# Performance work log

Hardware: AMD Instinct MI355X
Metric: run time of the kernel (lower is better)

## Reference

```python
import jax, jax.numpy as jnp
import numpy as np

V, L, H, D = 2048, 16, 8, 64   # vocab, max_chars, n_head, word_vec_d
B = 8192                        # number of words in batch (rows of char_code)
NW_TOTAL = 8192                 # len(word_code)
N_NAMES = 2048                  # total names (4 words each)
N_GROUPS = 8                    # groups of names (256 each)
PAD = 0
TEMP = D ** 0.5
LN_EPS = 1e-5


def make_pos():
    freq = D // 2
    inv = 1.0 / np.power(10000.0, np.arange(freq) / freq)
    ph = np.outer(np.arange(L), inv)
    return jnp.asarray(np.hstack([np.cos(ph), np.sin(ph)]).astype(np.float32))


def setup_inputs() -> dict:
    key = jax.random.key(0)
    ks = jax.random.split(key, 8)
    char_emb = jax.random.normal(ks[0], (V, D), jnp.float32) * 0.02
    char_emb = char_emb.at[PAD].set(0.0)  # padding_idx row
    Wc = jax.random.normal(ks[1], (D, 3 * H * D), jnp.float32) * 0.02
    bc = jnp.zeros((3 * H * D,), jnp.float32)
    Wp = jax.random.normal(ks[2], (D, 3 * H * D), jnp.float32) * 0.02
    bp = jnp.zeros((3 * H * D,), jnp.float32)
    gamma = jnp.ones((D,), jnp.float32)
    beta = jnp.zeros((D,), jnp.float32)
    W1 = jax.random.normal(ks[3], (H, 16), jnp.float32) * 0.1
    b1 = jnp.zeros((16,), jnp.float32)
    W2 = jax.random.normal(ks[4], (16, 8), jnp.float32) * 0.1
    b2 = jnp.zeros((8,), jnp.float32)
    char_code = jax.random.randint(ks[5], (B, L), 1, V)
    char_code = char_code.at[::4, -2:].set(PAD)  # some padded tails
    word_code = jax.random.randint(ks[6], (NW_TOTAL,), 0, B)
    n_words = np.full((N_NAMES,), NW_TOTAL // N_NAMES, dtype=np.int64)
    n_names = np.full((N_GROUPS,), N_NAMES // N_GROUPS, dtype=np.int64)
    return {"char_emb": char_emb, "Wc": Wc, "bc": bc, "Wp": Wp, "bp": bp,
            "gamma": gamma, "beta": beta, "W1": W1, "b1": b1, "W2": W2, "b2": b2,
            "char_code": char_code, "word_code": word_code,
            "n_words": n_words, "n_names": n_names}


def reference(char_emb, Wc, bc, Wp, bp, gamma, beta, W1, b1, W2, b2,
              char_code, word_code, n_words, n_names):
    pos = make_pos()
    # ComputeQKV: linear d -> 3*H*d, reshape [N,3,H,D]
    cqkv = (char_emb @ Wc + bc).reshape(V, 3, H, D)
    cq, ck, cv = cqkv[:, 0], cqkv[:, 1], cqkv[:, 2]        # [V,H,D]
    pqkv = (pos @ Wp + bp).reshape(L, 3, H, D)
    pq, pk, pv = pqkv[:, 0], pqkv[:, 1], pqkv[:, 2]        # [L,H,D]
    # precomputed score tables
    char_qk = jnp.einsum('xhd,yhd->hxy', cq, ck).at[:, :, PAD].set(-1e9)  # [H,V,V]
    pos_qk = jnp.einsum('xhd,yhd->hxy', pq, pk)                            # [H,L,L]
    # char_q@pos_k + (pos_q@char_k)^T summed over the first dim of char_pos_qk
    cp = jnp.einsum('vhd,lhd->hvl', cq, pk) + jnp.einsum('lhd,vhd->hvl', pq, ck)  # [H,V,L]
    code = char_code                                        # [B,L]
    # gather-assembled scores, no [H,B*L,V] intermediate
    sim = (char_qk[:, code[:, :, None], code[:, None, :]]   # [H,B,L,L]
           + cp[:, code]
           + pos_qk[:, None]) / TEMP
    attn = jax.nn.softmax(sim, axis=-1)                     # [H,B,L,L] (dropout=0)
    v = jnp.transpose(cv[code], (2, 0, 1, 3)) + pv.transpose(1, 0, 2)[:, None]  # [H,B,L,D]
    out = jnp.einsum('hbij,hbjd->bihd', attn, v)            # [B,L,H,D]
    mu = out.mean(-1, keepdims=True)
    var = out.var(-1, keepdims=True)
    out = (out - mu) / jnp.sqrt(var + LN_EPS) * gamma + beta  # LayerNorm(D)
    char_ft = jnp.transpose(out, (0, 2, 1, 3))              # [B,H,L,D]
    mask = (code != PAD)
    pooled = jnp.einsum('bl,bhld->bhd', mask.astype(out.dtype), char_ft) \
             / mask.sum(-1)[:, None, None]                  # masked mean over chars
    x = jnp.transpose(pooled, (0, 2, 1))                    # [B,D,H]
    x = jax.nn.relu(x @ W1 + b1) @ W2 + b2                  # MLP over head dim -> [B,D,8]
    word_ft = x.reshape(B, -1)[word_code]                   # [NW_TOTAL, D*8]
    nw = np.asarray(n_words)
    seg = jnp.asarray(np.repeat(np.arange(nw.size), nw))
    name_ft = jax.ops.segment_sum(word_ft, seg, num_segments=nw.size) \
              / jnp.asarray(nw, word_ft.dtype)[:, None]     # ragged mean -> [N_NAMES, D*8]
    splits = np.cumsum(np.asarray(n_names))[:-1]
    return tuple(jnp.split(name_ft, splits, axis=0))
```

## Files before the change

kernel.cpp:

```cpp
#include <hip/hip_runtime.h>
#include <hip/hip_bf16.h>
#include <math.h>

typedef __attribute__((ext_vector_type(8))) short bfrag;
typedef __attribute__((ext_vector_type(4))) float ffrag;
typedef __attribute__((ext_vector_type(4))) float f4v;
typedef __attribute__((ext_vector_type(2))) float f2v;

#define C3 1536
#define PS 24

__device__ __forceinline__ unsigned short f2bf(float f) {
    unsigned u = __float_as_uint(f);
    return (unsigned short)((u + 0x7FFFu + ((u >> 16) & 1u)) >> 16);
}
__device__ __forceinline__ float bf2f(unsigned short u) {
    return __uint_as_float((unsigned)u << 16);
}

__device__ __forceinline__ float row16_sum(float x) {
    int v;
    v = __builtin_amdgcn_update_dpp(0, __float_as_int(x), 0xB1, 0xF, 0xF, true);
    x += __int_as_float(v);
    v = __builtin_amdgcn_update_dpp(0, __float_as_int(x), 0x4E, 0xF, 0xF, true);
    x += __int_as_float(v);
    v = __builtin_amdgcn_update_dpp(0, __float_as_int(x), 0x124, 0xF, 0xF, true);
    x += __int_as_float(v);
    v = __builtin_amdgcn_update_dpp(0, __float_as_int(x), 0x128, 0xF, 0xF, true);
    x += __int_as_float(v);
    return x;
}

__global__ __launch_bounds__(256) void precompute_kernel(
    const float* __restrict__ char_emb, const float* __restrict__ Wc, const float* __restrict__ bc,
    const float* __restrict__ Wp, const float* __restrict__ bp,
    const float* __restrict__ gamma, const float* __restrict__ beta,
    unsigned short* __restrict__ cqkv, unsigned short* __restrict__ pbf,
    unsigned short* __restrict__ pvb, float* __restrict__ gbtab)
{
    const int b = blockIdx.x;
    const int t = threadIdx.x;
    if (b < 1536) {
        const int mt = b / 6;
        const int nt = b - mt * 6;
        const int m0 = mt * 8;
        const int c = nt * 256 + t;
        const float qs = (c < 512) ? 0.125f : 1.f;
        const float bias = bc[c];
        float acc[8];
        #pragma unroll
        for (int r = 0; r < 8; ++r) acc[r] = bias;
        #pragma unroll 16
        for (int dd = 0; dd < 64; ++dd) {
            const float wv = Wc[dd * C3 + c];
            #pragma unroll
            for (int r = 0; r < 8; ++r)
                acc[r] = fmaf(char_emb[(m0 + r) * 64 + dd], wv, acc[r]);
        }
        #pragma unroll
        for (int r = 0; r < 8; ++r)
            cqkv[(size_t)(m0 + r) * C3 + c] = f2bf(acc[r] * qs);
    } else {
        const int e = b - 1536;
        const int l = e / 6;
        const int cc = e - l * 6;
        if (b == 1536 && t < 64) {
            #pragma unroll
            for (int dt = 0; dt < 4; ++dt) {
                gbtab[t * 8 + dt]     = gamma[dt * 16 + t];
                gbtab[t * 8 + 4 + dt] = beta[dt * 16 + t];
            }
        }
        __shared__ float spos[64];
        if (t < 64) {
            const int f = t & 31;
            const float inv = exp2f(-(float)f * 0.41524101186092034f);
            const float ph = (float)l * inv;
            spos[t] = (t < 32) ? cosf(ph) : sinf(ph);
        }
        __syncthreads();
        const int c = t + cc * 256;
        float acc = bp[c];
        #pragma unroll
        for (int dd = 0; dd < 64; ++dd)
            acc = fmaf(spos[dd], Wp[dd * C3 + c], acc);
        if (c < 1024) {
            const float qs = (c < 512) ? 0.125f : 1.f;
            pbf[(c >> 6) * 1024 + l * 64 + (c & 63)] = f2bf(acc * qs);
        } else {
            const int h = (c >> 6) & 7, d = c & 63;
            pvb[((h * 4 + (d >> 4)) * 2 + (l >> 3)) * 128 + (d & 15) * 8 + (l & 7)] = f2bf(acc);
        }
    }
}

__global__ __launch_bounds__(256) void cp_kernel(
    const unsigned short* __restrict__ cqkv, const unsigned short* __restrict__ pbf,
    float* __restrict__ cps, float* __restrict__ pqk)
{
    const int b = blockIdx.x;
    const int t = threadIdx.x;
    if (b < 256) {
        const int lane = t & 63, wid = t >> 6;
        const int quad = lane >> 4, n = lane & 15;
        const int h = b >> 5;
        const int v0 = (b & 31) * 64 + wid * 16;
        const unsigned short* arow = cqkv + (size_t)(v0 + n) * C3 + h * 64;
        const unsigned short* pk = pbf + (8 + h) * 1024 + n * 64;
        const unsigned short* pq = pbf + h * 1024 + n * 64;
        ffrag acc = {0.f, 0.f, 0.f, 0.f};
        #pragma unroll
        for (int s = 0; s < 2; ++s) {
            const bfrag aF = *(const bfrag*)(arow + s * 32 + quad * 8);
            const bfrag bF = *(const bfrag*)(pk + s * 32 + quad * 8);
            acc = __builtin_amdgcn_mfma_f32_16x16x32_bf16(aF, bF, acc, 0, 0, 0);
        }
        #pragma unroll
        for (int s = 0; s < 2; ++s) {
            const bfrag aF = *(const bfrag*)(arow + 512 + s * 32 + quad * 8);
            const bfrag bF = *(const bfrag*)(pq + s * 32 + quad * 8);
            acc = __builtin_amdgcn_mfma_f32_16x16x32_bf16(aF, bF, acc, 0, 0, 0);
        }
        #pragma unroll
        for (int r = 0; r < 4; ++r)
            cps[((size_t)h * 2048 + v0 + quad * 4 + r) * 16 + n] = acc[r];
    } else {
        #pragma unroll
        for (int i = 0; i < 8; ++i) {
            const int e = t * 8 + i;
            const int h = e >> 8, r = (e >> 4) & 15, c = e & 15;
            const unsigned short* pq = pbf + h * 1024 + r * 64;
            const unsigned short* pk = pbf + (8 + h) * 1024 + c * 64;
            float s = 0.f;
            #pragma unroll
            for (int c8 = 0; c8 < 8; ++c8) {
                const bfrag a = *(const bfrag*)(pq + c8 * 8);
                const bfrag bb = *(const bfrag*)(pk + c8 * 8);
                #pragma unroll
                for (int j = 0; j < 8; ++j)
                    s += bf2f((unsigned short)a[j]) * bf2f((unsigned short)bb[j]);
            }
            pqk[e] = s;
        }
    }
}

__global__ __launch_bounds__(256, 5) void attn_kernel(
    const unsigned short* __restrict__ cqkv,
    const unsigned short* __restrict__ pvb, const int* __restrict__ char_code,
    const float* __restrict__ gbtab,
    const float* __restrict__ cps, const float* __restrict__ pqk,
    const float* __restrict__ W1, const float* __restrict__ b1,
    const float* __restrict__ W2, const float* __restrict__ b2,
    float* __restrict__ x)
{
    __shared__ __attribute__((aligned(16))) unsigned short sVt[4 * 1024];
    __shared__ __attribute__((aligned(16))) unsigned short sP[4 * 16 * PS];
    __shared__ float sPool[512];
    __shared__ float sHid[64 * 17];
    __shared__ float sWb[280];

    const int t = threadIdx.x;
    const int lane = t & 63;
    const int wid = t >> 6;
    const int w = blockIdx.x;
    const int quad = lane >> 4;
    const int n = lane & 15;
    const int q2 = quad & 1;

    if (t < 128) { sWb[t] = W1[t]; sWb[144 + t] = W2[t]; }
    else if (t < 144) sWb[t] = b1[t - 128];
    else if (t < 152) sWb[272 + (t - 144)] = b2[t - 144];

    const int code = char_code[w * 16 + n];
    const bool kvalid = (code != 0);
    const unsigned long long msk = __ballot(kvalid);
    const int nv = __popcll(msk & 0xFFFFull);

    int rc[4];
    #pragma unroll
    for (int rr = 0; rr < 4; ++rr) rc[rr] = __shfl(code, quad * 4 + rr);

    const f4v g4 = *(const f4v*)(gbtab + n * 8);
    const f4v b4 = *(const f4v*)(gbtab + n * 8 + 4);

    unsigned short* vt = sVt + wid * 1024;
    unsigned short* pt = sP + wid * 16 * PS;

    bfrag onesf;
    #pragma unroll
    for (int j = 0; j < 8; ++j) onesf[j] = (short)0x3F80;

    #pragma unroll
    for (int c2 = 0; c2 < 2; ++c2) {
        const int h = wid + c2 * 4;

        const unsigned short* cvp = cqkv + (size_t)code * C3 + 1024 + h * 64;
        #pragma unroll
        for (int cc = 0; cc < 2; ++cc) {
            const int d8 = quad + cc * 4;
            const bfrag cv = *(const bfrag*)(cvp + d8 * 8);
            #pragma unroll
            for (int j = 0; j < 8; ++j) {
                const int d = d8 * 8 + j;
                const int e = ((d >> 4) * 2 + (n >> 3)) * 128
                            + ((d & 15) ^ ((n >> 3) << 2)) * 8 + (n & 7);
                vt[e] = (unsigned short)cv[j];
            }
        }

        const float* cph = cps + (size_t)h * 32768;
        const float* pqh = pqk + h * 256;
        ffrag accS;
        #pragma unroll
        for (int rr = 0; rr < 4; ++rr)
            accS[rr] = cph[rc[rr] * 16 + n] + pqh[(quad * 4 + rr) * 16 + n];
        const unsigned short* cbase = cqkv + (size_t)code * C3 + h * 64;
        #pragma unroll
        for (int cc = 0; cc < 2; ++cc) {
            const int off = quad * 8 + cc * 32;
            const bfrag cqF = *(const bfrag*)(cbase + off);
            const bfrag ckF = *(const bfrag*)(cbase + 512 + off);
            accS = __builtin_amdgcn_mfma_f32_16x16x32_bf16(cqF, ckF, accS, 0, 0, 0);
        }

        #pragma unroll
        for (int r = 0; r < 4; ++r) {
            const float pr = kvalid ? __expf(accS[r]) : 0.f;
            pt[(quad * 4 + r) * PS + n] = f2bf(pr);
        }

        bfrag ap;
        #pragma unroll
        for (int j = 0; j < 8; ++j) ap[j] = 0;
        if (quad < 2) ap = *(const bfrag*)(pt + n * PS + quad * 8);
        ffrag accO[4];
        #pragma unroll
        for (int dt = 0; dt < 4; ++dt) { ffrag z = {0.f,0.f,0.f,0.f}; accO[dt] = z; }
        #pragma unroll
        for (int dt = 0; dt < 4; ++dt) {
            const bfrag bcv = *(const bfrag*)(vt + (dt * 2 + q2) * 128 + (n ^ (q2 << 2)) * 8);
            accO[dt] = __builtin_amdgcn_mfma_f32_16x16x32_bf16(ap, bcv, accO[dt], 0, 0, 0);
            const bfrag bpv = *(const bfrag*)(pvb + ((h * 4 + dt) * 2 + q2) * 128 + n * 8);
            accO[dt] = __builtin_amdgcn_mfma_f32_16x16x32_bf16(ap, bpv, accO[dt], 0, 0, 0);
        }
        ffrag accE = {0.f, 0.f, 0.f, 0.f};
        accE = __builtin_amdgcn_mfma_f32_16x16x32_bf16(ap, onesf, accE, 0, 0, 0);

        float ps1[4], ps2[4];
        #pragma unroll
        for (int r = 0; r < 4; ++r) {
            ps1[r] = accO[0][r] + accO[1][r] + accO[2][r] + accO[3][r];
            ps2[r] = accO[0][r]*accO[0][r] + accO[1][r]*accO[1][r]
                   + accO[2][r]*accO[2][r] + accO[3][r]*accO[3][r];
            ps1[r] = row16_sum(ps1[r]);
            ps2[r] = row16_sum(ps2[r]);
        }
        float pool[4] = {0.f, 0.f, 0.f, 0.f};
        #pragma unroll
        for (int r = 0; r < 4; ++r) {
            const float mu   = ps1[r] * 0.015625f;
            const float var  = fmaxf(ps2[r] * 0.015625f - mu * mu, 0.f);
            const float rstd = rsqrtf(var + accE[r] * accE[r] * 1e-5f);
            const float iv = ((msk >> (quad * 4 + r)) & 1ull) ? 1.f : 0.f;
            #pragma unroll
            for (int dt = 0; dt < 4; ++dt)
                pool[dt] += iv * fmaf((accO[dt][r] - mu) * rstd, g4[dt], b4[dt]);
        }
        #pragma unroll
        for (int xm = 16; xm <= 32; xm <<= 1) {
            #pragma unroll
            for (int dt = 0; dt < 4; ++dt) pool[dt] += __shfl_xor(pool[dt], xm);
        }
        if (quad == 0) {
            const float invnv = 1.f / (float)nv;
            #pragma unroll
            for (int dt = 0; dt < 4; ++dt)
                sPool[h * 64 + n * 4 + dt] = pool[dt] * invnv;
        }
    }
    __syncthreads();

    if (t < 64) {
        const int dmap = (t & 15) * 4 + (t >> 4);
        float pl[8];
        #pragma unroll
        for (int hh = 0; hh < 8; ++hh) pl[hh] = sPool[hh * 64 + dmap];
        #pragma unroll
        for (int c = 0; c < 16; ++c) {
            float hs = sWb[128 + c];
            #pragma unroll
            for (int hh = 0; hh < 8; ++hh) hs = fmaf(pl[hh], sWb[hh * 16 + c], hs);
            sHid[t * 17 + c] = fmaxf(hs, 0.f);
        }
    }
    __syncthreads();
    {
        const int d = t >> 2, o0 = (t & 3) * 2;
        float a0 = sWb[272 + o0], a1 = sWb[272 + o0 + 1];
        #pragma unroll
        for (int c = 0; c < 16; ++c) {
            const float hc = sHid[d * 17 + c];
            a0 = fmaf(hc, sWb[144 + c * 8 + o0], a0);
            a1 = fmaf(hc, sWb[144 + c * 8 + o0 + 1], a1);
        }
        f2v res; res[0] = a0; res[1] = a1;
        *(f2v*)(x + (size_t)w * 512 + t * 2) = res;
    }
}

__global__ __launch_bounds__(256) void name_avg_kernel(
    const float* __restrict__ x, const int* __restrict__ word_code,
    const int* __restrict__ n_words, float* __restrict__ out)
{
    const int t = threadIdx.x;
    const int lane = t & 63;
    const int nm = blockIdx.x * 4 + (t >> 6);

    int part = 0;
    for (int i = lane; i < nm; i += 64) part += n_words[i];
    #pragma unroll
    for (int xm = 1; xm <= 32; xm <<= 1) part += __shfl_xor(part, xm);
    const int off = part;
    const int cnt = n_words[nm];

    f4v a0 = {0.f,0.f,0.f,0.f}, a1 = {0.f,0.f,0.f,0.f};
    for (int r = 0; r < cnt; ++r) {
        const int wc = word_code[off + r];
        const f4v u0 = *(const f4v*)(x + (size_t)wc * 512 + lane * 8);
        const f4v u1 = *(const f4v*)(x + (size_t)wc * 512 + lane * 8 + 4);
        #pragma unroll
        for (int k = 0; k < 4; ++k) { a0[k] += u0[k]; a1[k] += u1[k]; }
    }
    const float inv = 1.f / (float)cnt;
    #pragma unroll
    for (int k = 0; k < 4; ++k) { a0[k] *= inv; a1[k] *= inv; }
    *(f4v*)(out + (size_t)nm * 512 + lane * 8) = a0;
    *(f4v*)(out + (size_t)nm * 512 + lane * 8 + 4) = a1;
}

extern "C" void kernel_launch(void* const* d_in, const int* in_sizes, int n_in,
                              void* d_out, int out_size, void* d_ws, size_t ws_size,
                              hipStream_t stream) {
    (void)in_sizes; (void)n_in; (void)out_size; (void)ws_size;
    const float* char_emb = (const float*)d_in[0];
    const float* Wc    = (const float*)d_in[1];
    const float* bc    = (const float*)d_in[2];
    const float* Wp    = (const float*)d_in[3];
    const float* bp    = (const float*)d_in[4];
    const float* gamma = (const float*)d_in[5];
    const float* beta  = (const float*)d_in[6];
    const float* W1    = (const float*)d_in[7];
    const float* b1    = (const float*)d_in[8];
    const float* W2    = (const float*)d_in[9];
    const float* b2    = (const float*)d_in[10];
    const int* char_code = (const int*)d_in[11];
    const int* word_code = (const int*)d_in[12];
    const int* n_words   = (const int*)d_in[13];

    char* ws = (char*)d_ws;
    unsigned short* cqkv = (unsigned short*)ws;
    unsigned short* pbf  = (unsigned short*)(ws + 6291456);
    unsigned short* pvb  = (unsigned short*)(ws + 6324224);
    float* x     = (float*)(ws + 6340608);
    float* gbtab = (float*)(ws + 23117824);
    float* cps   = (float*)(ws + 23119872);
    float* pqk   = (float*)(ws + 24168448);
    float* out = (float*)d_out;

    precompute_kernel<<<1632, 256, 0, stream>>>(char_emb, Wc, bc, Wp, bp, gamma, beta,
                                                cqkv, pbf, pvb, gbtab);
    cp_kernel<<<257, 256, 0, stream>>>(cqkv, pbf, cps, pqk);
    attn_kernel<<<8192, 256, 0, stream>>>(cqkv, pvb, char_code, gbtab, cps, pqk,
                                          W1, b1, W2, b2, x);
    name_avg_kernel<<<512, 256, 0, stream>>>(x, word_code, n_words, out);
}
```

Before: 186.1 us.

## Move per-word MLP from attention kernel into name-averaging gather kernel

The attention kernel now writes the pooled [8 heads x 64] features directly to global memory and no longer runs the two-layer head MLP. That removes two block barriers, the shared-memory weight staging and the extra LDS arrays from each of its 8192 blocks. The MLP now runs inside the name-averaging kernel on each gathered word, and W2 and b2 are applied after averaging using linearity. The trade-off is that every gathered word recomputes the MLP, and pooled values are read with strided per-lane loads instead of contiguous vector loads.

```diff
diff --git a/kernel.cpp b/kernel.cpp
--- a/kernel.cpp
+++ b/kernel.cpp
@@ -150,15 +150,10 @@
     const unsigned short* __restrict__ pvb, const int* __restrict__ char_code,
     const float* __restrict__ gbtab,
     const float* __restrict__ cps, const float* __restrict__ pqk,
-    const float* __restrict__ W1, const float* __restrict__ b1,
-    const float* __restrict__ W2, const float* __restrict__ b2,
-    float* __restrict__ x)
+    float* __restrict__ pooled)
 {
     __shared__ __attribute__((aligned(16))) unsigned short sVt[4 * 1024];
     __shared__ __attribute__((aligned(16))) unsigned short sP[4 * 16 * PS];
-    __shared__ float sPool[512];
-    __shared__ float sHid[64 * 17];
-    __shared__ float sWb[280];
 
     const int t = threadIdx.x;
     const int lane = t & 63;
@@ -168,10 +163,6 @@
     const int n = lane & 15;
     const int q2 = quad & 1;
 
-    if (t < 128) { sWb[t] = W1[t]; sWb[144 + t] = W2[t]; }
-    else if (t < 144) sWb[t] = b1[t - 128];
-    else if (t < 152) sWb[272 + (t - 144)] = b2[t - 144];
-
     const int code = char_code[w * 16 + n];
     const bool kvalid = (code != 0);
     const unsigned long long msk = __ballot(kvalid);
@@ -274,49 +265,31 @@
         }
         if (quad == 0) {
             const float invnv = 1.f / (float)nv;
-            #pragma unroll
-            for (int dt = 0; dt < 4; ++dt)
-                sPool[h * 64 + n * 4 + dt] = pool[dt] * invnv;
+            f4v res;
+            #pragma unroll
+            for (int dt = 0; dt < 4; ++dt) res[dt] = pool[dt] * invnv;
+            *(f4v*)(pooled + (size_t)w * 512 + h * 64 + n * 4) = res;
         }
     }
-    __syncthreads();
-
-    if (t < 64) {
-        const int dmap = (t & 15) * 4 + (t >> 4);
-        float pl[8];
-        #pragma unroll
-        for (int hh = 0; hh < 8; ++hh) pl[hh] = sPool[hh * 64 + dmap];
-        #pragma unroll
-        for (int c = 0; c < 16; ++c) {
-            float hs = sWb[128 + c];
-            #pragma unroll
-            for (int hh = 0; hh < 8; ++hh) hs = fmaf(pl[hh], sWb[hh * 16 + c], hs);
-            sHid[t * 17 + c] = fmaxf(hs, 0.f);
-        }
-    }
-    __syncthreads();
-    {
-        const int d = t >> 2, o0 = (t & 3) * 2;
-        float a0 = sWb[272 + o0], a1 = sWb[272 + o0 + 1];
-        #pragma unroll
-        for (int c = 0; c < 16; ++c) {
-            const float hc = sHid[d * 17 + c];
-            a0 = fmaf(hc, sWb[144 + c * 8 + o0], a0);
-            a1 = fmaf(hc, sWb[144 + c * 8 + o0 + 1], a1);
-        }
-        f2v res; res[0] = a0; res[1] = a1;
-        *(f2v*)(x + (size_t)w * 512 + t * 2) = res;
-    }
-}
-
-__global__ __launch_bounds__(256) void name_avg_kernel(
-    const float* __restrict__ x, const int* __restrict__ word_code,
-    const int* __restrict__ n_words, float* __restrict__ out)
+}
+
+__global__ __launch_bounds__(256) void name_mlp_avg_kernel(
+    const float* __restrict__ pooled, const int* __restrict__ word_code,
+    const int* __restrict__ n_words,
+    const float* __restrict__ W1, const float* __restrict__ b1,
+    const float* __restrict__ W2, const float* __restrict__ b2,
+    float* __restrict__ out)
 {
+    __shared__ float sWb[280];
     const int t = threadIdx.x;
     const int lane = t & 63;
     const int nm = blockIdx.x * 4 + (t >> 6);
 
+    if (t < 128) { sWb[t] = W1[t]; sWb[144 + t] = W2[t]; }
+    else if (t < 144) sWb[t] = b1[t - 128];
+    else if (t < 152) sWb[272 + (t - 144)] = b2[t - 144];
+    __syncthreads();
+
     int part = 0;
     for (int i = lane; i < nm; i += 64) part += n_words[i];
     #pragma unroll
@@ -324,19 +297,35 @@
     const int off = part;
     const int cnt = n_words[nm];
 
-    f4v a0 = {0.f,0.f,0.f,0.f}, a1 = {0.f,0.f,0.f,0.f};
+    const int pidx = (lane & 15) * 4 + (lane >> 4);
+    float a[8];
+    #pragma unroll
+    for (int o = 0; o < 8; ++o) a[o] = 0.f;
+
     for (int r = 0; r < cnt; ++r) {
         const int wc = word_code[off + r];
-        const f4v u0 = *(const f4v*)(x + (size_t)wc * 512 + lane * 8);
-        const f4v u1 = *(const f4v*)(x + (size_t)wc * 512 + lane * 8 + 4);
-        #pragma unroll
-        for (int k = 0; k < 4; ++k) { a0[k] += u0[k]; a1[k] += u1[k]; }
+        const float* pr = pooled + (size_t)wc * 512 + pidx;
+        float pl[8];
+        #pragma unroll
+        for (int hh = 0; hh < 8; ++hh) pl[hh] = pr[hh * 64];
+        #pragma unroll
+        for (int c = 0; c < 16; ++c) {
+            float hs = sWb[128 + c];
+            #pragma unroll
+            for (int hh = 0; hh < 8; ++hh) hs = fmaf(pl[hh], sWb[hh * 16 + c], hs);
+            hs = fmaxf(hs, 0.f);
+            #pragma unroll
+            for (int o = 0; o < 8; ++o) a[o] = fmaf(hs, sWb[144 + c * 8 + o], a[o]);
+        }
     }
     const float inv = 1.f / (float)cnt;
-    #pragma unroll
-    for (int k = 0; k < 4; ++k) { a0[k] *= inv; a1[k] *= inv; }
-    *(f4v*)(out + (size_t)nm * 512 + lane * 8) = a0;
-    *(f4v*)(out + (size_t)nm * 512 + lane * 8 + 4) = a1;
+    f4v r0, r1;
+    #pragma unroll
+    for (int o = 0; o < 4; ++o) { r0[o] = a[o] * inv + sWb[272 + o]; }
+    #pragma unroll
+    for (int o = 0; o < 4; ++o) { r1[o] = a[4 + o] * inv + sWb[276 + o]; }
+    *(f4v*)(out + (size_t)nm * 512 + lane * 8) = r0;
+    *(f4v*)(out + (size_t)nm * 512 + lane * 8 + 4) = r1;
 }
 
 extern "C" void kernel_launch(void* const* d_in, const int* in_sizes, int n_in,
@@ -362,7 +351,7 @@
     unsigned short* cqkv = (unsigned short*)ws;
     unsigned short* pbf  = (unsigned short*)(ws + 6291456);
     unsigned short* pvb  = (unsigned short*)(ws + 6324224);
-    float* x     = (float*)(ws + 6340608);
+    float* pooled = (float*)(ws + 6340608);
     float* gbtab = (float*)(ws + 23117824);
     float* cps   = (float*)(ws + 23119872);
     float* pqk   = (float*)(ws + 24168448);
@@ -371,7 +360,7 @@
     precompute_kernel<<<1632, 256, 0, stream>>>(char_emb, Wc, bc, Wp, bp, gamma, beta,
                                                 cqkv, pbf, pvb, gbtab);
     cp_kernel<<<257, 256, 0, stream>>>(cqkv, pbf, cps, pqk);
-    attn_kernel<<<8192, 256, 0, stream>>>(cqkv, pvb, char_code, gbtab, cps, pqk,
-                                          W1, b1, W2, b2, x);
-    name_avg_kernel<<<512, 256, 0, stream>>>(x, word_code, n_words, out);
-}
+    attn_kernel<<<8192, 256, 0, stream>>>(cqkv, pvb, char_code, gbtab, cps, pqk, pooled);
+    name_mlp_avg_kernel<<<512, 256, 0, stream>>>(pooled, word_code, n_words,
+                                                 W1, b1, W2, b2, out);
+}
```

Measured after the change: 194.4 us. 4.5% more time.
